# Optimization experiments

Hardware: AMD Instinct MI355X
Metric: run time of the kernel (lower is better)

Reference implementation:

```python
import jax, jax.numpy as jnp
import numpy as np

B, S, DM, H = 2, 2048, 1024, 16
D = DM // H
SCALE = D ** -0.5


def setup_inputs() -> dict:
    key = jax.random.key(0)
    k1, k2, k3 = jax.random.split(key, 3)
    x = jax.random.normal(k1, (B, S, DM), dtype=jnp.float32)
    w_qkv = jax.random.normal(k2, (DM, 3 * DM), dtype=jnp.float32) * (DM ** -0.5)
    b_qkv = jnp.zeros((3 * DM,), dtype=jnp.float32)
    w_out = jax.random.normal(k3, (DM, DM), dtype=jnp.float32) * (DM ** -0.5)
    b_out = jnp.zeros((DM,), dtype=jnp.float32)
    return {"x": x, "w_qkv": w_qkv, "b_qkv": b_qkv, "w_out": w_out, "b_out": b_out}


def reference(x, w_qkv, b_qkv, w_out, b_out):
    b, n, _ = x.shape
    qkv = x @ w_qkv + b_qkv                          # [b, n, 3*dm]
    q, k, v = jnp.split(qkv, 3, axis=-1)
    # b n (h d) -> b h n d
    split = lambda t: t.reshape(b, n, H, D).transpose(0, 2, 1, 3)
    q, k, v = split(q), split(k), split(v)
    dots = jnp.einsum('bhid,bhjd->bhij', q, k) * SCALE
    # causal (fore) mask: -inf above the diagonal
    causal = jnp.tril(jnp.ones((n, n), dtype=bool))
    dots = jnp.where(causal, dots, -jnp.inf)
    attn = jax.nn.softmax(dots, axis=-1)
    out = jnp.einsum('bhij,bhjd->bhid', attn, v)     # [b, h, n, d]
    out = out.transpose(0, 2, 1, 3).reshape(b, n, H * D)
    return out @ w_out + b_out
```

## Files before the change

kernel.cpp:

```cpp
#include <hip/hip_runtime.h>
#include <hip/hip_bf16.h>

#define NB 2
#define NS 2048
#define NDM 1024
#define NH 16
#define ND 64
#define NM (NB * NS)
#define SCALE 0.125f

typedef __attribute__((ext_vector_type(8))) short bf16x8;
typedef __attribute__((ext_vector_type(4))) float f32x4;

__device__ __forceinline__ unsigned short f2bf(float f) {
    unsigned int u = __float_as_uint(f);
    u += 0x7fffu + ((u >> 16) & 1u);
    return (unsigned short)(u >> 16);
}

__device__ __forceinline__ void gload16(const unsigned short* g, unsigned short* l) {
    __builtin_amdgcn_global_load_lds(
        (const __attribute__((address_space(1))) void*)g,
        (__attribute__((address_space(3))) void*)l, 16, 0, 0);
}

__global__ __launch_bounds__(256)
void convert_bf16(const float* __restrict__ in, unsigned short* __restrict__ out, int n8) {
    int i = blockIdx.x * 256 + threadIdx.x;
    const int stride = gridDim.x * 256;
    for (; i < n8; i += stride) {
        const float4 a = ((const float4*)in)[i * 2];
        const float4 b = ((const float4*)in)[i * 2 + 1];
        bf16x8 v;
        v[0] = (short)f2bf(a.x); v[1] = (short)f2bf(a.y);
        v[2] = (short)f2bf(a.z); v[3] = (short)f2bf(a.w);
        v[4] = (short)f2bf(b.x); v[5] = (short)f2bf(b.y);
        v[6] = (short)f2bf(b.z); v[7] = (short)f2bf(b.w);
        *(bf16x8*)(out + (size_t)i * 8) = v;
    }
}

__global__ __launch_bounds__(256)
void transpose_bf16(const float* __restrict__ W, unsigned short* __restrict__ WT,
                    int K, int N) {
    __shared__ float Ts[64][65];
    const int n0 = blockIdx.x * 64, k0 = blockIdx.y * 64;
    const int t = threadIdx.x;
    {
        const int c4 = (t & 15) * 4;
        #pragma unroll
        for (int p = 0; p < 4; p++) {
            const int r = (t >> 4) + p * 16;
            const float4 v = *(const float4*)(W + (size_t)(k0 + r) * N + n0 + c4);
            Ts[r][c4] = v.x; Ts[r][c4 + 1] = v.y; Ts[r][c4 + 2] = v.z; Ts[r][c4 + 3] = v.w;
        }
    }
    __syncthreads();
    {
        const int cc8 = (t & 7) * 8;
        #pragma unroll
        for (int p = 0; p < 2; p++) {
            const int rr = (t >> 3) + p * 32;
            bf16x8 v;
            #pragma unroll
            for (int j = 0; j < 8; j++) v[j] = (short)f2bf(Ts[cc8 + j][rr]);
            *(bf16x8*)(WT + (size_t)(n0 + rr) * K + k0 + cc8) = v;
        }
    }
}

template<int MODE>
__global__ __launch_bounds__(256)
void gemm128(const unsigned short* __restrict__ A, const unsigned short* __restrict__ BT,
             const float* __restrict__ bias, void* __restrict__ Cv,
             unsigned short* __restrict__ qH, unsigned short* __restrict__ kH,
             unsigned short* __restrict__ vT,
             int M, int N, int K) {
    __shared__ unsigned short As[128 * 32];
    __shared__ unsigned short Bs[128 * 32];

    const int t = threadIdx.x, lane = t & 63, wv = t >> 6;
    const int wm = wv >> 1, wn = wv & 1;
    const int m0 = blockIdx.y * 128, n0 = blockIdx.x * 128;
    const int fr = lane & 15, fg = lane >> 4;

    f32x4 acc[4][4];
    #pragma unroll
    for (int m = 0; m < 4; m++)
        #pragma unroll
        for (int n = 0; n < 4; n++)
            #pragma unroll
            for (int r = 0; r < 4; r++) acc[m][n][r] = 0.f;

    for (int k0 = 0; k0 < K; k0 += 32) {
        __syncthreads();
        #pragma unroll
        for (int i = 0; i < 2; i++) {
            const int u = t + i * 256;
            const int row = u >> 2;
            const int grp = (u & 3) ^ ((row ^ (row >> 2)) & 3);
            unsigned short* ldsA = &As[(i * 256 + wv * 64) * 8];
            unsigned short* ldsB = &Bs[(i * 256 + wv * 64) * 8];
            gload16(A  + (size_t)(m0 + row) * K + k0 + grp * 8, ldsA);
            gload16(BT + (size_t)(n0 + row) * K + k0 + grp * 8, ldsB);
        }
        __syncthreads();

        bf16x8 af[4], bfv[4];
        #pragma unroll
        for (int m = 0; m < 4; m++) {
            const int row = wm * 64 + m * 16 + fr;
            const int g = fg ^ ((row ^ (row >> 2)) & 3);
            af[m] = *(const bf16x8*)&As[row * 32 + g * 8];
        }
        #pragma unroll
        for (int n = 0; n < 4; n++) {
            const int row = wn * 64 + n * 16 + fr;
            const int g = fg ^ ((row ^ (row >> 2)) & 3);
            bfv[n] = *(const bf16x8*)&Bs[row * 32 + g * 8];
        }
        #pragma unroll
        for (int m = 0; m < 4; m++)
            #pragma unroll
            for (int n = 0; n < 4; n++)
                acc[m][n] = __builtin_amdgcn_mfma_f32_16x16x32_bf16(
                    af[m], bfv[n], acc[m][n], 0, 0, 0);
    }

    const int lg = lane >> 4;
    #pragma unroll
    for (int m = 0; m < 4; m++)
        #pragma unroll
        for (int n = 0; n < 4; n++) {
            const int col = n0 + wn * 64 + n * 16 + fr;
            const float bb = bias[col];
            #pragma unroll
            for (int rg = 0; rg < 4; rg++) {
                const int row = m0 + wm * 64 + m * 16 + lg * 4 + rg;
                const float v = acc[m][n][rg] + bb;
                if (MODE == 0) {
                    ((float*)Cv)[(size_t)row * N + col] = v;
                } else {
                    const int part = col >> 10;
                    const int h = (col >> 6) & 15, d = col & 63;
                    const int bb2 = row >> 11, s = row & (NS - 1);
                    const size_t bh = (size_t)bb2 * NH + h;
                    const unsigned short bf = f2bf(v);
                    if (part == 0)      qH[(bh * NS + s) * ND + d] = bf;
                    else if (part == 1) kH[(bh * NS + s) * ND + d] = bf;
                    else                vT[(bh * ND + d) * NS + s] = bf;
                }
            }
        }
}

__global__ __launch_bounds__(256)
void attn_mfma(const unsigned short* __restrict__ qH, const unsigned short* __restrict__ kH,
               const unsigned short* __restrict__ vT, unsigned short* __restrict__ atto) {
    const int bx = blockIdx.x;
    const int qt = (NS / 64 - 1) - (bx >> 5);
    const int bh = bx & 31;
    const int h = bh & (NH - 1), b = bh >> 4;
    const int q0 = qt * 64;
    const int t = threadIdx.x, lane = t & 63, wv = t >> 6;
    const int fr = lane & 15, fg = lane >> 4;
    const int fk = fg * 8;

    __shared__ unsigned short Kt[128 * 64];
    __shared__ unsigned short Vt[64 * 128];
    __shared__ unsigned short Ps[4][16 * 128];

    const unsigned short* kb = kH + (size_t)bh * NS * ND;
    const unsigned short* vb = vT + (size_t)bh * ND * NS;

    bf16x8 qf[2];
    {
        const unsigned short* qrow = qH + ((size_t)bh * NS + q0 + wv * 16 + fr) * ND;
        qf[0] = *(const bf16x8*)(qrow + fk);
        qf[1] = *(const bf16x8*)(qrow + 32 + fk);
    }

    f32x4 oacc[4];
    #pragma unroll
    for (int d = 0; d < 4; d++)
        #pragma unroll
        for (int r = 0; r < 4; r++) oacc[d][r] = 0.f;
    float mrow[4] = {-INFINITY, -INFINITY, -INFINITY, -INFINITY};
    float lrow[4] = {0.f, 0.f, 0.f, 0.f};

    const int ntiles = (qt >> 1) + 1;
    for (int jt = 0; jt < ntiles; jt++) {
        __syncthreads();
        #pragma unroll
        for (int i = 0; i < 4; i++) {
            const int u = t + i * 256;
            const int row = u >> 3;
            const int grp = (u & 7) ^ (row & 7);
            gload16(kb + (size_t)(jt * 128 + row) * ND + grp * 8,
                    &Kt[(i * 256 + wv * 64) * 8]);
        }
        #pragma unroll
        for (int i = 0; i < 4; i++) {
            const int u = t + i * 256;
            const int row = u >> 4;
            const int grp = (u & 15) ^ (row & 7);
            gload16(vb + (size_t)row * NS + jt * 128 + grp * 8,
                    &Vt[(i * 256 + wv * 64) * 8]);
        }
        __syncthreads();

        f32x4 sacc[8];
        #pragma unroll
        for (int kbi = 0; kbi < 8; kbi++) {
            #pragma unroll
            for (int r = 0; r < 4; r++) sacc[kbi][r] = 0.f;
            const int row = kbi * 16 + fr;
            const int g0 = (fg)     ^ (row & 7);
            const int g1 = (4 + fg) ^ (row & 7);
            const bf16x8 kf0 = *(const bf16x8*)&Kt[row * 64 + g0 * 8];
            const bf16x8 kf1 = *(const bf16x8*)&Kt[row * 64 + g1 * 8];
            sacc[kbi] = __builtin_amdgcn_mfma_f32_16x16x32_bf16(qf[0], kf0, sacc[kbi], 0, 0, 0);
            sacc[kbi] = __builtin_amdgcn_mfma_f32_16x16x32_bf16(qf[1], kf1, sacc[kbi], 0, 0, 0);
        }
        #pragma unroll
        for (int kbi = 0; kbi < 8; kbi++)
            #pragma unroll
            for (int r = 0; r < 4; r++) sacc[kbi][r] *= SCALE;

        if (jt == ntiles - 1) {
            #pragma unroll
            for (int kbi = 0; kbi < 8; kbi++) {
                const int keyg = jt * 128 + kbi * 16 + fr;
                #pragma unroll
                for (int reg = 0; reg < 4; reg++) {
                    const int qg = q0 + wv * 16 + fg * 4 + reg;
                    if (keyg > qg) sacc[kbi][reg] = -INFINITY;
                }
            }
        }

        float alpha[4];
        #pragma unroll
        for (int reg = 0; reg < 4; reg++) {
            float pm = sacc[0][reg];
            #pragma unroll
            for (int kbi = 1; kbi < 8; kbi++) pm = fmaxf(pm, sacc[kbi][reg]);
            pm = fmaxf(pm, __shfl_xor(pm, 1));
            pm = fmaxf(pm, __shfl_xor(pm, 2));
            pm = fmaxf(pm, __shfl_xor(pm, 4));
            pm = fmaxf(pm, __shfl_xor(pm, 8));
            const float mn = fmaxf(mrow[reg], pm);
            alpha[reg] = __expf(mrow[reg] - mn);
            mrow[reg] = mn;
            float ps = 0.f;
            #pragma unroll
            for (int kbi = 0; kbi < 8; kbi++) {
                const float p = __expf(sacc[kbi][reg] - mn);
                sacc[kbi][reg] = p;
                ps += p;
            }
            ps += __shfl_xor(ps, 1);
            ps += __shfl_xor(ps, 2);
            ps += __shfl_xor(ps, 4);
            ps += __shfl_xor(ps, 8);
            lrow[reg] = lrow[reg] * alpha[reg] + ps;
        }

        #pragma unroll
        for (int kbi = 0; kbi < 8; kbi++) {
            const int colk = kbi * 16 + fr;
            #pragma unroll
            for (int reg = 0; reg < 4; reg++) {
                const int prow = fg * 4 + reg;
                const int g = ((colk >> 3) ^ (prow & 7));
                Ps[wv][prow * 128 + g * 8 + (colk & 7)] = f2bf(sacc[kbi][reg]);
            }
        }
        #pragma unroll
        for (int dblk = 0; dblk < 4; dblk++)
            #pragma unroll
            for (int reg = 0; reg < 4; reg++) oacc[dblk][reg] *= alpha[reg];

        bf16x8 pf[4];
        #pragma unroll
        for (int ks = 0; ks < 4; ks++) {
            const int g = (ks * 4 + fg) ^ (fr & 7);
            pf[ks] = *(const bf16x8*)&Ps[wv][fr * 128 + g * 8];
        }
        #pragma unroll
        for (int dblk = 0; dblk < 4; dblk++) {
            const int vrow = dblk * 16 + fr;
            #pragma unroll
            for (int ks = 0; ks < 4; ks++) {
                const int g = (ks * 4 + fg) ^ (vrow & 7);
                const bf16x8 vf = *(const bf16x8*)&Vt[vrow * 128 + g * 8];
                oacc[dblk] = __builtin_amdgcn_mfma_f32_16x16x32_bf16(
                    pf[ks], vf, oacc[dblk], 0, 0, 0);
            }
        }
    }

    #pragma unroll
    for (int reg = 0; reg < 4; reg++) {
        const float inv = 1.f / lrow[reg];
        const int row = q0 + wv * 16 + fg * 4 + reg;
        unsigned short* dst = atto + ((size_t)b * NS + row) * NDM + h * ND;
        #pragma unroll
        for (int dblk = 0; dblk < 4; dblk++)
            dst[dblk * 16 + fr] = f2bf(oacc[dblk][reg] * inv);
    }
}

extern "C" void kernel_launch(void* const* d_in, const int* in_sizes, int n_in,
                              void* d_out, int out_size, void* d_ws, size_t ws_size,
                              hipStream_t stream) {
    const float* x     = (const float*)d_in[0];
    const float* w_qkv = (const float*)d_in[1];
    const float* b_qkv = (const float*)d_in[2];
    const float* w_out = (const float*)d_in[3];
    const float* b_out = (const float*)d_in[4];
    float* out = (float*)d_out;

    unsigned short* xb   = (unsigned short*)d_ws;
    unsigned short* wqT  = xb   + (size_t)NM * NDM;
    unsigned short* woT  = wqT  + (size_t)3 * NDM * NDM;
    unsigned short* qH   = woT  + (size_t)NDM * NDM;
    unsigned short* kH   = qH   + (size_t)NM * NDM;
    unsigned short* vT   = kH   + (size_t)NM * NDM;
    unsigned short* atto = vT   + (size_t)NM * NDM;

    convert_bf16<<<2048, 256, 0, stream>>>(x, xb, NM * NDM / 8);
    transpose_bf16<<<dim3(3 * NDM / 64, NDM / 64), 256, 0, stream>>>(w_qkv, wqT, NDM, 3 * NDM);
    transpose_bf16<<<dim3(NDM / 64, NDM / 64), 256, 0, stream>>>(w_out, woT, NDM, NDM);

    gemm128<1><<<dim3(3 * NDM / 128, NM / 128), 256, 0, stream>>>(
        xb, wqT, b_qkv, nullptr, qH, kH, vT, NM, 3 * NDM, NDM);

    attn_mfma<<<dim3((NS / 64) * NB * NH), 256, 0, stream>>>(qH, kH, vT, atto);

    gemm128<0><<<dim3(NDM / 128, NM / 128), 256, 0, stream>>>(
        atto, woT, b_out, out, nullptr, nullptr, nullptr, NM, NDM, NDM);
}
```

Measured before the change: 214.2 us.

## Double-buffer attention K/V tiles, write row-major QKV, add V transpose kernel

The QKV GEMM epilogue now writes a plain row-major bf16 qkv buffer instead of scattered per-head Q/K and transposed V stores, and a separate vtrans kernel builds the transposed V. The attention kernel moves to 64-key tiles with double-buffered LDS staging so the next tile loads while the current one computes. It also folds the scale into exp2 with a lazy-rescale threshold that skips the rescale when the row max barely grows, and raises wave priority around the MFMA blocks. The aim is to remove uncoalesced epilogue stores and global-load latency in attention, at the cost of an extra kernel launch and more loop iterations.

```diff
diff --git a/kernel.cpp b/kernel.cpp
--- a/kernel.cpp
+++ b/kernel.cpp
@@ -7,7 +7,9 @@
 #define NH 16
 #define ND 64
 #define NM (NB * NS)
-#define SCALE 0.125f
+#define RS 3072
+#define C1 0.1803368801111243f
+#define THR_RAW 44.36141956f
 
 typedef __attribute__((ext_vector_type(8))) short bf16x8;
 typedef __attribute__((ext_vector_type(4))) float f32x4;
@@ -69,12 +71,42 @@
     }
 }
 
+__global__ __launch_bounds__(256)
+void vtrans(const unsigned short* __restrict__ qkvb, unsigned short* __restrict__ vT) {
+    __shared__ unsigned short Ts[64][65];
+    const int st = blockIdx.x, bh = blockIdx.y;
+    const int h = bh & (NH - 1), b = bh >> 4;
+    const int t = threadIdx.x;
+    {
+        const int c8 = (t & 7) * 8;
+        #pragma unroll
+        for (int p = 0; p < 2; p++) {
+            const int r = (t >> 3) + p * 32;
+            const unsigned short* src =
+                qkvb + (size_t)(b * NS + st * 64 + r) * RS + 2 * NDM + h * ND + c8;
+            const bf16x8 v = *(const bf16x8*)src;
+            #pragma unroll
+            for (int j = 0; j < 8; j++) Ts[r][c8 + j] = (unsigned short)v[j];
+        }
+    }
+    __syncthreads();
+    {
+        #pragma unroll
+        for (int i = 0; i < 2; i++) {
+            const int u = t + i * 256;
+            const int d = u >> 3, cg = (u & 7) * 8;
+            bf16x8 v;
+            #pragma unroll
+            for (int j = 0; j < 8; j++) v[j] = (short)Ts[cg + j][d];
+            *(bf16x8*)(vT + ((size_t)bh * ND + d) * NS + st * 64 + cg) = v;
+        }
+    }
+}
+
 template<int MODE>
 __global__ __launch_bounds__(256)
 void gemm128(const unsigned short* __restrict__ A, const unsigned short* __restrict__ BT,
              const float* __restrict__ bias, void* __restrict__ Cv,
-             unsigned short* __restrict__ qH, unsigned short* __restrict__ kH,
-             unsigned short* __restrict__ vT,
              int M, int N, int K) {
     __shared__ unsigned short As[128 * 32];
     __shared__ unsigned short Bs[128 * 32];
@@ -99,10 +131,8 @@
             const int u = t + i * 256;
             const int row = u >> 2;
             const int grp = (u & 3) ^ ((row ^ (row >> 2)) & 3);
-            unsigned short* ldsA = &As[(i * 256 + wv * 64) * 8];
-            unsigned short* ldsB = &Bs[(i * 256 + wv * 64) * 8];
-            gload16(A  + (size_t)(m0 + row) * K + k0 + grp * 8, ldsA);
-            gload16(BT + (size_t)(n0 + row) * K + k0 + grp * 8, ldsB);
+            gload16(A  + (size_t)(m0 + row) * K + k0 + grp * 8, &As[(i * 256 + wv * 64) * 8]);
+            gload16(BT + (size_t)(n0 + row) * K + k0 + grp * 8, &Bs[(i * 256 + wv * 64) * 8]);
         }
         __syncthreads();
 
@@ -110,14 +140,12 @@
         #pragma unroll
         for (int m = 0; m < 4; m++) {
             const int row = wm * 64 + m * 16 + fr;
-            const int g = fg ^ ((row ^ (row >> 2)) & 3);
-            af[m] = *(const bf16x8*)&As[row * 32 + g * 8];
+            af[m] = *(const bf16x8*)&As[row * 32 + (fg ^ ((row ^ (row >> 2)) & 3)) * 8];
         }
         #pragma unroll
         for (int n = 0; n < 4; n++) {
             const int row = wn * 64 + n * 16 + fr;
-            const int g = fg ^ ((row ^ (row >> 2)) & 3);
-            bfv[n] = *(const bf16x8*)&Bs[row * 32 + g * 8];
+            bfv[n] = *(const bf16x8*)&Bs[row * 32 + (fg ^ ((row ^ (row >> 2)) & 3)) * 8];
         }
         #pragma unroll
         for (int m = 0; m < 4; m++)
@@ -127,7 +155,6 @@
                     af[m], bfv[n], acc[m][n], 0, 0, 0);
     }
 
-    const int lg = lane >> 4;
     #pragma unroll
     for (int m = 0; m < 4; m++)
         #pragma unroll
@@ -136,27 +163,17 @@
             const float bb = bias[col];
             #pragma unroll
             for (int rg = 0; rg < 4; rg++) {
-                const int row = m0 + wm * 64 + m * 16 + lg * 4 + rg;
+                const int row = m0 + wm * 64 + m * 16 + fg * 4 + rg;
                 const float v = acc[m][n][rg] + bb;
-                if (MODE == 0) {
-                    ((float*)Cv)[(size_t)row * N + col] = v;
-                } else {
-                    const int part = col >> 10;
-                    const int h = (col >> 6) & 15, d = col & 63;
-                    const int bb2 = row >> 11, s = row & (NS - 1);
-                    const size_t bh = (size_t)bb2 * NH + h;
-                    const unsigned short bf = f2bf(v);
-                    if (part == 0)      qH[(bh * NS + s) * ND + d] = bf;
-                    else if (part == 1) kH[(bh * NS + s) * ND + d] = bf;
-                    else                vT[(bh * ND + d) * NS + s] = bf;
-                }
-            }
-        }
-}
-
-__global__ __launch_bounds__(256)
-void attn_mfma(const unsigned short* __restrict__ qH, const unsigned short* __restrict__ kH,
-               const unsigned short* __restrict__ vT, unsigned short* __restrict__ atto) {
+                if (MODE == 0) ((float*)Cv)[(size_t)row * N + col] = v;
+                else ((unsigned short*)Cv)[(size_t)row * N + col] = f2bf(v);
+            }
+        }
+}
+
+__global__ __launch_bounds__(256)
+void attn_mfma(const unsigned short* __restrict__ qkvb, const unsigned short* __restrict__ vT,
+               unsigned short* __restrict__ atto) {
     const int bx = blockIdx.x;
     const int qt = (NS / 64 - 1) - (bx >> 5);
     const int bh = bx & 31;
@@ -164,20 +181,20 @@
     const int q0 = qt * 64;
     const int t = threadIdx.x, lane = t & 63, wv = t >> 6;
     const int fr = lane & 15, fg = lane >> 4;
-    const int fk = fg * 8;
-
-    __shared__ unsigned short Kt[128 * 64];
-    __shared__ unsigned short Vt[64 * 128];
-    __shared__ unsigned short Ps[4][16 * 128];
-
-    const unsigned short* kb = kH + (size_t)bh * NS * ND;
+
+    __shared__ unsigned short Kt[2][64 * 64];
+    __shared__ unsigned short Vt[2][64 * 64];
+    __shared__ unsigned short Ps[4][16 * 64];
+
+    const unsigned short* kb = qkvb + (size_t)b * NS * RS + NDM + h * ND;
     const unsigned short* vb = vT + (size_t)bh * ND * NS;
 
     bf16x8 qf[2];
     {
-        const unsigned short* qrow = qH + ((size_t)bh * NS + q0 + wv * 16 + fr) * ND;
-        qf[0] = *(const bf16x8*)(qrow + fk);
-        qf[1] = *(const bf16x8*)(qrow + 32 + fk);
+        const unsigned short* qrow =
+            qkvb + (size_t)(b * NS + q0 + wv * 16 + fr) * RS + h * ND;
+        qf[0] = *(const bf16x8*)(qrow + fg * 8);
+        qf[1] = *(const bf16x8*)(qrow + 32 + fg * 8);
     }
 
     f32x4 oacc[4];
@@ -186,51 +203,56 @@
         #pragma unroll
         for (int r = 0; r < 4; r++) oacc[d][r] = 0.f;
     float mrow[4] = {-INFINITY, -INFINITY, -INFINITY, -INFINITY};
+    float nmC[4]  = {INFINITY, INFINITY, INFINITY, INFINITY};
     float lrow[4] = {0.f, 0.f, 0.f, 0.f};
 
-    const int ntiles = (qt >> 1) + 1;
+    const int ntiles = qt + 1;
+
+#define STAGE_KV(cbuf, jtile)                                                        \
+    {                                                                                \
+        _Pragma("unroll")                                                            \
+        for (int i = 0; i < 2; i++) {                                                \
+            const int u = t + i * 256;                                               \
+            const int row = u >> 3;                                                  \
+            const int grp = (u & 7) ^ (row & 7);                                     \
+            gload16(kb + (size_t)((jtile) * 64 + row) * RS + grp * 8,                \
+                    &Kt[cbuf][(i * 256 + wv * 64) * 8]);                             \
+        }                                                                            \
+        _Pragma("unroll")                                                            \
+        for (int i = 0; i < 2; i++) {                                                \
+            const int u = t + i * 256;                                               \
+            const int row = u >> 3;                                                  \
+            const int grp = (u & 7) ^ (row & 7);                                     \
+            gload16(vb + (size_t)row * NS + (jtile) * 64 + grp * 8,                  \
+                    &Vt[cbuf][(i * 256 + wv * 64) * 8]);                             \
+        }                                                                            \
+    }
+
+    STAGE_KV(0, 0);
+
     for (int jt = 0; jt < ntiles; jt++) {
+        const int cur = jt & 1;
         __syncthreads();
-        #pragma unroll
-        for (int i = 0; i < 4; i++) {
-            const int u = t + i * 256;
-            const int row = u >> 3;
-            const int grp = (u & 7) ^ (row & 7);
-            gload16(kb + (size_t)(jt * 128 + row) * ND + grp * 8,
-                    &Kt[(i * 256 + wv * 64) * 8]);
-        }
-        #pragma unroll
-        for (int i = 0; i < 4; i++) {
-            const int u = t + i * 256;
-            const int row = u >> 4;
-            const int grp = (u & 15) ^ (row & 7);
-            gload16(vb + (size_t)row * NS + jt * 128 + grp * 8,
-                    &Vt[(i * 256 + wv * 64) * 8]);
-        }
-        __syncthreads();
-
-        f32x4 sacc[8];
-        #pragma unroll
-        for (int kbi = 0; kbi < 8; kbi++) {
+        if (jt + 1 < ntiles) STAGE_KV(cur ^ 1, jt + 1);
+
+        f32x4 sacc[4];
+        __builtin_amdgcn_s_setprio(1);
+        #pragma unroll
+        for (int kbi = 0; kbi < 4; kbi++) {
             #pragma unroll
             for (int r = 0; r < 4; r++) sacc[kbi][r] = 0.f;
             const int row = kbi * 16 + fr;
-            const int g0 = (fg)     ^ (row & 7);
-            const int g1 = (4 + fg) ^ (row & 7);
-            const bf16x8 kf0 = *(const bf16x8*)&Kt[row * 64 + g0 * 8];
-            const bf16x8 kf1 = *(const bf16x8*)&Kt[row * 64 + g1 * 8];
+            const bf16x8 kf0 = *(const bf16x8*)&Kt[cur][row * 64 + ((fg) ^ (row & 7)) * 8];
+            const bf16x8 kf1 = *(const bf16x8*)&Kt[cur][row * 64 + ((4 + fg) ^ (row & 7)) * 8];
             sacc[kbi] = __builtin_amdgcn_mfma_f32_16x16x32_bf16(qf[0], kf0, sacc[kbi], 0, 0, 0);
             sacc[kbi] = __builtin_amdgcn_mfma_f32_16x16x32_bf16(qf[1], kf1, sacc[kbi], 0, 0, 0);
         }
-        #pragma unroll
-        for (int kbi = 0; kbi < 8; kbi++)
-            #pragma unroll
-            for (int r = 0; r < 4; r++) sacc[kbi][r] *= SCALE;
+        __builtin_amdgcn_s_setprio(0);
 
         if (jt == ntiles - 1) {
             #pragma unroll
-            for (int kbi = 0; kbi < 8; kbi++) {
-                const int keyg = jt * 128 + kbi * 16 + fr;
+            for (int kbi = 0; kbi < 4; kbi++) {
+                const int keyg = jt * 64 + kbi * 16 + fr;
                 #pragma unroll
                 for (int reg = 0; reg < 4; reg++) {
                     const int qg = q0 + wv * 16 + fg * 4 + reg;
@@ -239,23 +261,38 @@
             }
         }
 
-        float alpha[4];
+        float pmax[4];
         #pragma unroll
         for (int reg = 0; reg < 4; reg++) {
-            float pm = sacc[0][reg];
-            #pragma unroll
-            for (int kbi = 1; kbi < 8; kbi++) pm = fmaxf(pm, sacc[kbi][reg]);
+            float pm = fmaxf(fmaxf(sacc[0][reg], sacc[1][reg]),
+                             fmaxf(sacc[2][reg], sacc[3][reg]));
             pm = fmaxf(pm, __shfl_xor(pm, 1));
             pm = fmaxf(pm, __shfl_xor(pm, 2));
             pm = fmaxf(pm, __shfl_xor(pm, 4));
             pm = fmaxf(pm, __shfl_xor(pm, 8));
-            const float mn = fmaxf(mrow[reg], pm);
-            alpha[reg] = __expf(mrow[reg] - mn);
-            mrow[reg] = mn;
+            pmax[reg] = pm;
+        }
+        bool need = false;
+        #pragma unroll
+        for (int reg = 0; reg < 4; reg++) need |= (pmax[reg] > mrow[reg] + THR_RAW);
+        if (__any(need)) {
+            #pragma unroll
+            for (int reg = 0; reg < 4; reg++) {
+                const float mn = fmaxf(mrow[reg], pmax[reg]);
+                const float alpha = __builtin_amdgcn_exp2f((mrow[reg] - mn) * C1);
+                mrow[reg] = mn;
+                nmC[reg] = -mn * C1;
+                lrow[reg] *= alpha;
+                #pragma unroll
+                for (int dblk = 0; dblk < 4; dblk++) oacc[dblk][reg] *= alpha;
+            }
+        }
+        #pragma unroll
+        for (int reg = 0; reg < 4; reg++) {
             float ps = 0.f;
             #pragma unroll
-            for (int kbi = 0; kbi < 8; kbi++) {
-                const float p = __expf(sacc[kbi][reg] - mn);
+            for (int kbi = 0; kbi < 4; kbi++) {
+                const float p = __builtin_amdgcn_exp2f(fmaf(sacc[kbi][reg], C1, nmC[reg]));
                 sacc[kbi][reg] = p;
                 ps += p;
             }
@@ -263,42 +300,39 @@
             ps += __shfl_xor(ps, 2);
             ps += __shfl_xor(ps, 4);
             ps += __shfl_xor(ps, 8);
-            lrow[reg] = lrow[reg] * alpha[reg] + ps;
-        }
-
-        #pragma unroll
-        for (int kbi = 0; kbi < 8; kbi++) {
+            lrow[reg] += ps;
+        }
+
+        #pragma unroll
+        for (int kbi = 0; kbi < 4; kbi++) {
             const int colk = kbi * 16 + fr;
             #pragma unroll
             for (int reg = 0; reg < 4; reg++) {
                 const int prow = fg * 4 + reg;
-                const int g = ((colk >> 3) ^ (prow & 7));
-                Ps[wv][prow * 128 + g * 8 + (colk & 7)] = f2bf(sacc[kbi][reg]);
-            }
-        }
-        #pragma unroll
-        for (int dblk = 0; dblk < 4; dblk++)
-            #pragma unroll
-            for (int reg = 0; reg < 4; reg++) oacc[dblk][reg] *= alpha[reg];
-
-        bf16x8 pf[4];
-        #pragma unroll
-        for (int ks = 0; ks < 4; ks++) {
-            const int g = (ks * 4 + fg) ^ (fr & 7);
-            pf[ks] = *(const bf16x8*)&Ps[wv][fr * 128 + g * 8];
-        }
+                Ps[wv][prow * 64 + (((colk >> 3) ^ (prow & 7)) << 3) + (colk & 7)] =
+                    f2bf(sacc[kbi][reg]);
+            }
+        }
+
+        bf16x8 pf[2];
+        #pragma unroll
+        for (int ks = 0; ks < 2; ks++)
+            pf[ks] = *(const bf16x8*)&Ps[wv][fr * 64 + ((ks * 4 + fg) ^ (fr & 7)) * 8];
+        __builtin_amdgcn_s_setprio(1);
         #pragma unroll
         for (int dblk = 0; dblk < 4; dblk++) {
             const int vrow = dblk * 16 + fr;
             #pragma unroll
-            for (int ks = 0; ks < 4; ks++) {
-                const int g = (ks * 4 + fg) ^ (vrow & 7);
-                const bf16x8 vf = *(const bf16x8*)&Vt[vrow * 128 + g * 8];
+            for (int ks = 0; ks < 2; ks++) {
+                const bf16x8 vf =
+                    *(const bf16x8*)&Vt[cur][vrow * 64 + ((ks * 4 + fg) ^ (vrow & 7)) * 8];
                 oacc[dblk] = __builtin_amdgcn_mfma_f32_16x16x32_bf16(
                     pf[ks], vf, oacc[dblk], 0, 0, 0);
             }
         }
-    }
+        __builtin_amdgcn_s_setprio(0);
+    }
+#undef STAGE_KV
 
     #pragma unroll
     for (int reg = 0; reg < 4; reg++) {
@@ -324,20 +358,21 @@
     unsigned short* xb   = (unsigned short*)d_ws;
     unsigned short* wqT  = xb   + (size_t)NM * NDM;
     unsigned short* woT  = wqT  + (size_t)3 * NDM * NDM;
-    unsigned short* qH   = woT  + (size_t)NDM * NDM;
-    unsigned short* kH   = qH   + (size_t)NM * NDM;
-    unsigned short* vT   = kH   + (size_t)NM * NDM;
-    unsigned short* atto = vT   + (size_t)NM * NDM;
+    unsigned short* qkvb = woT  + (size_t)NDM * NDM;
+    unsigned short* vT   = qkvb + (size_t)NM * 3 * NDM;
+    unsigned short* atto = xb;
 
     convert_bf16<<<2048, 256, 0, stream>>>(x, xb, NM * NDM / 8);
     transpose_bf16<<<dim3(3 * NDM / 64, NDM / 64), 256, 0, stream>>>(w_qkv, wqT, NDM, 3 * NDM);
     transpose_bf16<<<dim3(NDM / 64, NDM / 64), 256, 0, stream>>>(w_out, woT, NDM, NDM);
 
     gemm128<1><<<dim3(3 * NDM / 128, NM / 128), 256, 0, stream>>>(
-        xb, wqT, b_qkv, nullptr, qH, kH, vT, NM, 3 * NDM, NDM);
-
-    attn_mfma<<<dim3((NS / 64) * NB * NH), 256, 0, stream>>>(qH, kH, vT, atto);
+        xb, wqT, b_qkv, qkvb, NM, 3 * NDM, NDM);
+
+    vtrans<<<dim3(NS / 64, NB * NH), 256, 0, stream>>>(qkvb, vT);
+
+    attn_mfma<<<dim3((NS / 64) * NB * NH), 256, 0, stream>>>(qkvb, vT, atto);
 
     gemm128<0><<<dim3(NDM / 128, NM / 128), 256, 0, stream>>>(
-        atto, woT, b_out, out, nullptr, nullptr, nullptr, NM, NDM, NDM);
-}
+        atto, woT, b_out, out, NM, NDM, NDM);
+}
```

After: 215.5 us. Within noise of the previous version (+0.6%).
